# Optimization experiments

Hardware: AMD Instinct MI355X
Metric: run time of the kernel (lower is better)

The kernel has to match this reference:

```python
import jax, jax.numpy as jnp
import numpy as np

N = 50000      # areaNum
E = 64         # embeddingsize
NE = 800000    # nonzeros of normalized adjacency
WK = 9         # walk_length + 1
L = 2          # args.L
TMP = 0.5      # args.choosing_tmp
BIAS = 1e-4


def _logistic_noise(k, shape):
    # eps ~ U(bias, 1-bias); noise = log(eps) - log(1-eps)
    u = jax.random.uniform(k, shape, minval=BIAS, maxval=1.0 - BIAS)
    return jnp.log(u) - jnp.log1p(-u)


def setup_inputs() -> dict:
    key = jax.random.key(0)
    ks = jax.random.split(key, 16)
    rng = np.random.default_rng(0)

    # ---- normalized sparse adjacency (D^-1/2 A D^-1/2), COO sorted by row ----
    row = np.sort(rng.integers(0, N, NE))
    col = rng.integers(0, N, NE)
    deg = np.bincount(row, minlength=N).astype(np.float32)
    dinv = np.where(deg > 0, deg ** -0.5, 0.0).astype(np.float32)
    vals = dinv[row] * dinv[col]

    # ---- random-walk mean-pooling adjacency, row-normalized ----
    rw_row = np.repeat(np.arange(N), WK)
    rw_col = rng.integers(0, N, N * WK)
    rw_col[::WK] = np.arange(N)  # walk starts at self
    rw_vals = np.full(N * WK, 1.0 / WK, dtype=np.float32)

    def lin(k, fan_in, shape):
        return jax.random.normal(k, shape, dtype=jnp.float32) / np.sqrt(fan_in)

    inp = {
        'x': jax.random.normal(ks[0], (N, E), dtype=jnp.float32),
        'vals': jnp.asarray(vals),
        'rw_vals': jnp.asarray(rw_vals),
        't_W1': lin(ks[1], 2 * E, (L, 2 * E, E)),
        't_b1': jnp.zeros((L, E), jnp.float32),
        't_W2': lin(ks[2], E, (L, E, 1)),
        't_b2': jnp.zeros((L, 1), jnp.float32),
        's_W1': lin(ks[3], E, (L, E, E)),
        's_b1': jnp.zeros((L, E), jnp.float32),
        's_W2': lin(ks[4], E, (L, E, 1)),
        's_b2': jnp.zeros((L, 1), jnp.float32),
        't_noise': _logistic_noise(ks[5], (L, NE)),
        's_noise': _logistic_noise(ks[6], (L, N, 1)),
        'row': jnp.asarray(row, dtype=jnp.int64) if jax.config.jax_enable_x64 else jnp.asarray(row, dtype=jnp.int32),
        'col': jnp.asarray(col, dtype=jnp.int32),
        'rw_row': jnp.asarray(rw_row, dtype=jnp.int32),
        'rw_col': jnp.asarray(rw_col, dtype=jnp.int32),
    }
    inp['row'] = jnp.asarray(row, dtype=jnp.int32)
    return inp


def reference(x, vals, rw_vals, t_W1, t_b1, t_W2, t_b2, s_W1, s_b1, s_W2, s_b2,
              t_noise, s_noise, row, col, rw_row, rw_col):
    n = x.shape[0]

    def spmm(r, c, v, h):  # sparse [n,n] @ dense [n,E]
        return jax.ops.segment_sum(v[:, None] * h[c], r, num_segments=n)

    # per-edge concat of ORIGINAL embeddings (same tensor every layer, as in source)
    t_cat = jnp.concatenate([x[row], x[col]], axis=-1)  # [nE, 2E]

    # --- mask-learning pass ---
    cur = x
    t_masks, s_masks = [], []
    for i in range(L):
        cur = spmm(row, col, vals, cur)
        t_h = jax.nn.relu(t_cat @ t_W1[i] + t_b1[i])
        t_logit = t_h @ t_W2[i] + t_b2[i]                      # [nE,1]
        t_m = jax.nn.sigmoid((t_noise[i][:, None] + t_logit) / TMP)[:, 0]
        t_masks.append(t_m)
        s_h = jax.nn.relu(cur @ s_W1[i] + s_b1[i])
        s_logit = s_h @ s_W2[i] + s_b2[i]                      # [N,1]
        s_masks.append(jax.nn.sigmoid((s_noise[i] + s_logit) / TMP))

    # --- t branch: gated spmm propagation, mean over layers ---
    cur_t = x
    acc_t = x
    for i in range(L):
        cur_t = spmm(row, col, vals * t_masks[i], cur_t)
        acc_t = acc_t + cur_t
    emb_t = acc_t / (L + 1)

    # --- s branch: gated mix with random-walk mean pooling, then spmm ---
    cur_s = x
    acc_s = x
    s_reg = jnp.float32(0.0)
    for i in range(L):
        mp = spmm(rw_row, rw_col, rw_vals, cur_s)
        cur_s = s_masks[i] * cur_s + (1.0 - s_masks[i]) * mp
        cur_s = spmm(row, col, vals, cur_s)
        acc_s = acc_s + cur_s
        s_reg = s_reg + s_masks[i].sum() / n
    emb_s = acc_s / (L + 1)
    s_reg = s_reg / L
    t_reg = jnp.float32(0.0)  # source never accumulates into t_reg
    return emb_t, emb_s, t_reg, s_reg, t_masks[-1]
```

## Files before the change

kernel.cpp:

```cpp
#include <hip/hip_runtime.h>

#define NNODES 50000
#define EDIM 64
#define WKLEN 9
#define NEDGE 800000
#define NPAD (NNODES + 64)

using bf16x8 = __attribute__((ext_vector_type(8))) __bf16;
using f32x4  = __attribute__((ext_vector_type(4))) float;

__device__ __align__(256) unsigned short g_xbf[NPAD * EDIM];
__device__ __align__(256) unsigned short g_ABh[NNODES * 128];
__device__ __align__(256) unsigned short g_c1h[NPAD * EDIM];
__device__ __align__(256) unsigned short g_c2h[NPAD * EDIM];
__device__ __align__(256) unsigned short g_g0h[NNODES * EDIM];
__device__ __align__(256) unsigned short g_sc1h[NNODES * EDIM];
__device__ __align__(256) unsigned short g_Pr[NNODES * 128];
__device__ __align__(256) unsigned short g_Pc[NNODES * 128];
__device__ __align__(256) float g_mt0[NEDGE];
__device__ __align__(256) float g_mt1[NEDGE];
__device__ __align__(256) float g_sm0[NNODES];
__device__ __align__(256) float g_sm1[NNODES];
__device__ __align__(256) int   g_rowptr[NNODES + 1];
__device__ __align__(256) unsigned short g_Tswz[2048 * 8];
__device__ __align__(256) unsigned short g_Sswz[1024 * 8];

__device__ __forceinline__ unsigned short f2bf(float f) {
    union { float f; unsigned int i; } v;
    v.f = f;
    unsigned int r = v.i + 0x7FFFu + ((v.i >> 16) & 1u);
    return (unsigned short)(r >> 16);
}
__device__ __forceinline__ float bf2f_lo(unsigned int u) {
    union { unsigned int i; float f; } v; v.i = u << 16; return v.f;
}
__device__ __forceinline__ float bf2f_hi(unsigned int u) {
    union { unsigned int i; float f; } v; v.i = u & 0xFFFF0000u; return v.f;
}

__global__ __launch_bounds__(256) void misc_kernel(
    const float* __restrict__ x, const float* __restrict__ tW1,
    const float* __restrict__ sW1, const int* __restrict__ row,
    int n, int nE)
{
    int bid = blockIdx.x, tid = threadIdx.x;
    if (bid < 1563) {
        int i = bid * 256 + tid;
        if (i < NNODES * EDIM / 8) {
            const float* src = x + i * 8;
            union { unsigned short s[8]; uint4 q; } u;
#pragma unroll
            for (int j = 0; j < 8; ++j) u.s[j] = f2bf(src[j]);
            *(uint4*)&g_xbf[i * 8] = u.q;
        }
    } else if (bid < 1759) {
        int i = (bid - 1563) * 256 + tid;
        if (i > n) return;
        int lo = 0, hi = nE;
        while (lo < hi) {
            int mid = (lo + hi) >> 1;
            if (row[mid] < i) lo = mid + 1; else hi = mid;
        }
        g_rowptr[i] = lo;
    } else if (bid < 1767) {
        int t = (bid - 1759) * 256 + tid;
        int s = t >> 9, f = (t >> 6) & 7, ln = t & 63;
        int li = s >> 1, half = s & 1, ks = f >> 2, nn = f & 3;
        int q = ln >> 4, mcl = ln & 15;
        union { unsigned short sv[8]; uint4 q4; } u;
#pragma unroll
        for (int j = 0; j < 8; ++j) {
            int kg = half * 64 + ks * 32 + q * 8 + j;
            u.sv[j] = f2bf(tW1[li * 8192 + kg * 64 + nn * 16 + mcl]);
        }
        *(uint4*)&g_Tswz[t * 8] = u.q4;
    } else {
        int t = (bid - 1767) * 256 + tid;
        int li = t >> 9, ks = (t >> 8) & 1, nn = (t >> 6) & 3, ln = t & 63;
        int q = ln >> 4, mcl = ln & 15;
        union { unsigned short sv[8]; uint4 q4; } u;
#pragma unroll
        for (int j = 0; j < 8; ++j)
            u.sv[j] = f2bf(sW1[li * 4096 + (ks * 32 + q * 8 + j) * 64 + nn * 16 + mcl]);
        *(uint4*)&g_Sswz[t * 8] = u.q4;
    }
}

__global__ __launch_bounds__(256) void prep2_kernel(int n)
{
// ... 70 lines not shown
        float hB = fmaxf(bf2f_hi(r0[k]) + bf2f_hi(c0[k]) + b1_0[2 * k + 1], 0.f);
        p0 = fmaf(hA, w2_0[2 * k], p0);
        p0 = fmaf(hB, w2_0[2 * k + 1], p0);
        float gA = fmaxf(bf2f_lo(r1[k]) + bf2f_lo(c1[k]) + b1_1[2 * k], 0.f);
        float gB = fmaxf(bf2f_hi(r1[k]) + bf2f_hi(c1[k]) + b1_1[2 * k + 1], 0.f);
        p1 = fmaf(gA, w2_1[2 * k], p1);
        p1 = fmaf(gB, w2_1[2 * k + 1], p1);
    }
#pragma unroll
    for (int off = 1; off <= 4; off <<= 1) {
        p0 += __shfl_xor(p0, off, 64);
        p1 += __shfl_xor(p1, off, 64);
    }
    if (sub == 0) {
        float z0 = (tnoise[e] + p0 + tb2[0]) * 2.0f;
        float m0 = 1.0f / (1.0f + expf(-z0));
        g_mt0[e] = m0;
        float z1 = (tnoise[nE + e] + p1 + tb2[1]) * 2.0f;
        float m1 = 1.0f / (1.0f + expf(-z1));
        g_mt1[e] = m1;
        mask_out[e] = m1;
    }
}

__device__ __forceinline__ void nm_body(
    int bid, const unsigned short* __restrict__ cur, int li,
    const float* __restrict__ b1, const float* __restrict__ W2,
    const float* __restrict__ b2, const float* __restrict__ noise,
    float* __restrict__ smout, int n)
{
    int tid = threadIdx.x;
    int wave = tid >> 6, lane = tid & 63;
    int mc = lane & 15, quad = lane >> 4;
    int nb = bid * 64 + wave * 16;
    const unsigned short* basep = cur + (nb + mc) * 64 + quad * 8;
    bf16x8 af0 = *(const bf16x8*)basep;
    bf16x8 af1 = *(const bf16x8*)(basep + 32);
    f32x4 acc[4];
    const f32x4 zero = {0.f, 0.f, 0.f, 0.f};
#pragma unroll
    for (int nn = 0; nn < 4; ++nn) acc[nn] = zero;
#pragma unroll
    for (int nn = 0; nn < 4; ++nn) {
        bf16x8 b0 = *(const bf16x8*)&g_Sswz[((li * 8 + nn) * 64 + lane) * 8];
        bf16x8 b1f = *(const bf16x8*)&g_Sswz[((li * 8 + 4 + nn) * 64 + lane) * 8];
        acc[nn] = __builtin_amdgcn_mfma_f32_16x16x32_bf16(af0, b0, acc[nn], 0, 0, 0);
        acc[nn] = __builtin_amdgcn_mfma_f32_16x16x32_bf16(af1, b1f, acc[nn], 0, 0, 0);
    }
    float p[4];
#pragma unroll
    for (int r = 0; r < 4; ++r) {
        float s = 0.f;
#pragma unroll
        for (int nn = 0; nn < 4; ++nn) {
            float h = acc[nn][r] + b1[nn * 16 + mc];
            s = fmaf(fmaxf(h, 0.f), W2[nn * 16 + mc], s);
        }
        p[r] = s;
    }
#pragma unroll
    for (int off = 8; off >= 1; off >>= 1)
#pragma unroll
        for (int r = 0; r < 4; ++r) p[r] += __shfl_xor(p[r], off, 64);
    if (mc == 0) {
        float b2v = b2[0];
#pragma unroll
        for (int r = 0; r < 4; ++r) {
            int node = nb + quad * 4 + r;
            if (node < n) {
                float z = (noise[node] + p[r] + b2v) * 2.0f;
                smout[node] = 1.0f / (1.0f + expf(-z));
            }
        }
    }
}

__global__ __launch_bounds__(256) void nm0_kernel(
    const float* __restrict__ sb1, const float* __restrict__ sW2,
    const float* __restrict__ sb2, const float* __restrict__ snz, int n)
{
    nm_body(blockIdx.x, g_c1h, 0, sb1, sW2, sb2, snz, g_sm0, n);
}

__device__ __forceinline__ void s1_process16(
    int sb, int d2, int myc, float myv, float myvm,
    float& p0, float& p1, float& q0, float& q1)
{
    int cc[16]; float vv[16], mm[16]; unsigned uu[16];
#pragma unroll
    for (int k = 0; k < 16; ++k) {
        cc[k] = __shfl(myc, sb + k, 64);
        vv[k] = __shfl(myv, sb + k, 64);
        mm[k] = __shfl(myvm, sb + k, 64);
    }
#pragma unroll
    for (int k = 0; k < 16; ++k)
        uu[k] = *(const unsigned*)&g_xbf[cc[k] * 64 + 2 * d2];
#pragma unroll
    for (int k = 0; k < 16; ++k) {
        p0 = fmaf(vv[k], bf2f_lo(uu[k]), p0);
        p1 = fmaf(vv[k], bf2f_hi(uu[k]), p1);
        q0 = fmaf(mm[k], bf2f_lo(uu[k]), q0);
        q1 = fmaf(mm[k], bf2f_hi(uu[k]), q1);
    }
}

__global__ __launch_bounds__(256) void s1_kernel(
    const int* __restrict__ colv, const float* __restrict__ vals, int n)
{
    int half = threadIdx.x >> 5;
    int w = blockIdx.x * 8 + half;
    int el = half & 1;
    int d2 = threadIdx.x & 31;
    int sb0 = el << 5;
    int s = g_rowptr[w], e = g_rowptr[w + 1];
    float p0 = 0.f, p1 = 0.f, q0 = 0.f, q1 = 0.f;
    for (int base = s; base < e; base += 32) {
        int rem = e - base;
        int myc = 0; float myv = 0.f, myvm = 0.f;
        if (d2 < rem) {
            myc = colv[base + d2];
            myv = vals[base + d2];
            myvm = myv * g_mt0[base + d2];
        }
        s1_process16(sb0, d2, myc, myv, myvm, p0, p1, q0, q1);
        if (rem > 16)
            s1_process16(sb0 + 16, d2, myc, myv, myvm, p0, p1, q0, q1);
    }
    uint2 pk;
    pk.x = (unsigned)f2bf(p0) | ((unsigned)f2bf(q0) << 16);
    pk.y = (unsigned)f2bf(p1) | ((unsigned)f2bf(q1) << 16);
    *(uint2*)&g_ABh[w * 128 + 4 * d2] = pk;
    *(unsigned*)&g_c1h[w * 64 + 2 * d2] =
        (unsigned)f2bf(p0) | ((unsigned)f2bf(p1) << 16);
}

__device__ __forceinline__ void s2_process8(
    int sb, int d2, int myc, float myv, float myvm,
    float& c0, float& c1, float& t0, float& t1)
{
    int cc[8]; float vv[8], mm[8]; uint2 uu[8];
#pragma unroll
    for (int k = 0; k < 8; ++k) {
        cc[k] = __shfl(myc, sb + k, 64);
        vv[k] = __shfl(myv, sb + k, 64);
        mm[k] = __shfl(myvm, sb + k, 64);
    }
#pragma unroll
    for (int k = 0; k < 8; ++k)
        uu[k] = *(const uint2*)&g_ABh[cc[k] * 128 + 4 * d2];
#pragma unroll
    for (int k = 0; k < 8; ++k) {
        c0 = fmaf(vv[k], bf2f_lo(uu[k].x), c0);
        t0 = fmaf(mm[k], bf2f_hi(uu[k].x), t0);
        c1 = fmaf(vv[k], bf2f_lo(uu[k].y), c1);
        t1 = fmaf(mm[k], bf2f_hi(uu[k].y), t1);
    }
}

__device__ __forceinline__ void rw_body(
    int bid, const int* __restrict__ rw_col, const float* __restrict__ rwv,
    const unsigned short* __restrict__ cur, const float* __restrict__ smask,
    unsigned short* __restrict__ outg)
{
    int w = bid * 8 + (threadIdx.x >> 5);
    int d2 = threadIdx.x & 31;
    int base = w * WKLEN;
    float a0 = 0.f, a1 = 0.f;
#pragma unroll
    for (int j = 0; j < WKLEN; ++j) {
        int c = rw_col[base + j];
        float v = rwv[base + j];
        unsigned u = *(const unsigned*)&cur[c * 64 + 2 * d2];
        a0 = fmaf(v, bf2f_lo(u), a0);
        a1 = fmaf(v, bf2f_hi(u), a1);
    }
    float sm = smask[w];
    unsigned u = *(const unsigned*)&cur[w * 64 + 2 * d2];
    float r0 = sm * bf2f_lo(u) + (1.f - sm) * a0;
    float r1 = sm * bf2f_hi(u) + (1.f - sm) * a1;
    *(unsigned*)&outg[w * 64 + 2 * d2] =
        (unsigned)f2bf(r0) | ((unsigned)f2bf(r1) << 16);
}

__global__ __launch_bounds__(256) void s2_rw0_kernel(
    const int* __restrict__ colv, const float* __restrict__ vals,
    const int* __restrict__ rw_col, const float* __restrict__ rwv,
    const float* __restrict__ x, float* __restrict__ emb_t, int n)
{
    if (blockIdx.x >= 6250) {
        rw_body(blockIdx.x - 6250, rw_col, rwv, g_xbf, g_sm0, g_g0h);
        return;
    }
    int half = threadIdx.x >> 5;
    int w = blockIdx.x * 8 + half;
    int el = half & 1;
    int d2 = threadIdx.x & 31;
    int sb0 = el << 5;
    int s = g_rowptr[w], e = g_rowptr[w + 1];
    float c0 = 0.f, c1 = 0.f, t0 = 0.f, t1 = 0.f;
    for (int base = s; base < e; base += 32) {
        int rem = e - base;
        int myc = 0; float myv = 0.f, myvm = 0.f;
        if (d2 < rem) {
            myc = colv[base + d2];
            myv = vals[base + d2];
            myvm = myv * g_mt1[base + d2];
        }
        s2_process8(sb0, d2, myc, myv, myvm, c0, c1, t0, t1);
        if (rem > 8)  s2_process8(sb0 + 8,  d2, myc, myv, myvm, c0, c1, t0, t1);
        if (rem > 16) s2_process8(sb0 + 16, d2, myc, myv, myvm, c0, c1, t0, t1);
        if (rem > 24) s2_process8(sb0 + 24, d2, myc, myv, myvm, c0, c1, t0, t1);
    }
    int o2 = w * 64 + 2 * d2;
    uint2 U2v = *(const uint2*)&g_ABh[w * 128 + 4 * d2];
    float2 et;
    et.x = (x[o2]     + bf2f_hi(U2v.x) + t0) * (1.0f / 3.0f);
    et.y = (x[o2 + 1] + bf2f_hi(U2v.y) + t1) * (1.0f / 3.0f);
    *(float2*)&emb_t[o2] = et;
    *(unsigned*)&g_c2h[o2] = (unsigned)f2bf(c0) | ((unsigned)f2bf(c1) << 16);
}

__device__ __forceinline__ void sp_process16(
    const unsigned short* __restrict__ h, int sb, int d2,
    int myc, float myv, float& a0, float& a1)
{
    int cc[16]; float vv[16]; unsigned uu[16];
#pragma unroll
    for (int k = 0; k < 16; ++k) {
        cc[k] = __shfl(myc, sb + k, 64);
        vv[k] = __shfl(myv, sb + k, 64);
    }
#pragma unroll
    for (int k = 0; k < 16; ++k)
        uu[k] = *(const unsigned*)&h[cc[k] * 64 + 2 * d2];
#pragma unroll
    for (int k = 0; k < 16; ++k) {
        a0 = fmaf(vv[k], bf2f_lo(uu[k]), a0);
        a1 = fmaf(vv[k], bf2f_hi(uu[k]), a1);
    }
}

__device__ __forceinline__ void spmm_body(
    int bid, const int* __restrict__ colv, const float* __restrict__ vals,
    const unsigned short* __restrict__ h, float* __restrict__ l0,
    float* __restrict__ l1, int* __restrict__ wout, int* __restrict__ d2out)
{
    int half = threadIdx.x >> 5;
    int w = bid * 8 + half;
    int el = half & 1;
    int d2 = threadIdx.x & 31;
    int sb0 = el << 5;
    int s = g_rowptr[w], e = g_rowptr[w + 1];
    float a0 = 0.f, a1 = 0.f;
    for (int base = s; base < e; base += 32) {
        int rem = e - base;
        int myc = 0; float myv = 0.f;
        if (d2 < rem) {
            myc = colv[base + d2];
            myv = vals[base + d2];
        }
        sp_process16(h, sb0, d2, myc, myv, a0, a1);
        if (rem > 16) sp_process16(h, sb0 + 16, d2, myc, myv, a0, a1);
    }
    *l0 = a0; *l1 = a1; *wout = w; *d2out = d2;
}

__global__ __launch_bounds__(256) void spmm10_nm1_kernel(
    const int* __restrict__ colv, const float* __restrict__ vals,
    const float* __restrict__ sb1, const float* __restrict__ sW2,
    const float* __restrict__ sb2, const float* __restrict__ snz, int n)
{
    if (blockIdx.x >= 6250) {
        nm_body(blockIdx.x - 6250, g_c2h, 1, sb1, sW2, sb2, snz, g_sm1, n);
        return;
    }
    float a0, a1; int w, d2;
    spmm_body(blockIdx.x, colv, vals, g_g0h, &a0, &a1, &w, &d2);
    *(unsigned*)&g_sc1h[w * 64 + 2 * d2] =
        (unsigned)f2bf(a0) | ((unsigned)f2bf(a1) << 16);
}

__global__ __launch_bounds__(256) void rw1_kernel(
    const int* __restrict__ rw_col, const float* __restrict__ rwv)
{
    rw_body(blockIdx.x, rw_col, rwv, g_sc1h, g_sm1, g_g0h);
}

__global__ __launch_bounds__(256) void spmm12_fin_kernel(
    const int* __restrict__ colv, const float* __restrict__ vals,
    const float* __restrict__ x, float* __restrict__ emb_s,
    float* __restrict__ out, int n)
{
    if (blockIdx.x >= 6250) {
        __shared__ float red[256];
        float s = 0.f;
        for (int i = threadIdx.x; i < n; i += 256) s += g_sm0[i] + g_sm1[i];
        red[threadIdx.x] = s;
        __syncthreads();
        for (int off = 128; off >= 1; off >>= 1) {
            if (threadIdx.x < off) red[threadIdx.x] += red[threadIdx.x + off];
            __syncthreads();
        }
        if (threadIdx.x == 0) {
            out[6400000] = 0.0f;
            out[6400001] = red[0] / (2.0f * n);
        }
        return;
    }
    float a0, a1; int w, d2;
    spmm_body(blockIdx.x, colv, vals, g_g0h, &a0, &a1, &w, &d2);
    int o2 = w * 64 + 2 * d2;
    unsigned uc = *(const unsigned*)&g_sc1h[o2];
    float2 es;
    es.x = (x[o2]     + bf2f_lo(uc) + a0) * (1.0f / 3.0f);
    es.y = (x[o2 + 1] + bf2f_hi(uc) + a1) * (1.0f / 3.0f);
    *(float2*)&emb_s[o2] = es;
}

extern "C" void kernel_launch(void* const* d_in, const int* in_sizes, int n_in,
                              void* d_out, int out_size, void* d_ws, size_t ws_size,
                              hipStream_t stream)
{
    const float* x    = (const float*)d_in[0];
    const float* vals = (const float*)d_in[1];
    const float* rwv  = (const float*)d_in[2];
    const float* tW1  = (const float*)d_in[3];
    const float* tb1  = (const float*)d_in[4];
    const float* tW2  = (const float*)d_in[5];
    const float* tb2  = (const float*)d_in[6];
    const float* sW1  = (const float*)d_in[7];
    const float* sb1  = (const float*)d_in[8];
    const float* sW2  = (const float*)d_in[9];
    const float* sb2  = (const float*)d_in[10];
    const float* tnz  = (const float*)d_in[11];
    const float* snz  = (const float*)d_in[12];
    const int* row   = (const int*)d_in[13];
    const int* colv  = (const int*)d_in[14];
    const int* rwcol = (const int*)d_in[16];

    const int n = NNODES;
    const int nE = in_sizes[1];

    float* out   = (float*)d_out;
    float* emb_t = out;
    float* emb_s = out + 3200000;
    float* masko = out + 6400002;

    misc_kernel<<<1771, 256, 0, stream>>>(x, tW1, sW1, row, n, nE);
    prep2_kernel<<<782, 256, 0, stream>>>(n);
    edge_mask_kernel<<<nE / 32, 256, 0, stream>>>(tb1, tW2, tb2, tnz,
                                                  row, colv, masko, nE);
    s1_kernel<<<6250, 256, 0, stream>>>(colv, vals, n);
    nm0_kernel<<<782, 256, 0, stream>>>(sb1, sW2, sb2, snz, n);
    s2_rw0_kernel<<<12500, 256, 0, stream>>>(colv, vals, rwcol, rwv, x, emb_t, n);
    spmm10_nm1_kernel<<<6250 + 782, 256, 0, stream>>>(colv, vals,
                                                      sb1 + 64, sW2 + 64, sb2 + 1,
                                                      snz + n, n);
    rw1_kernel<<<6250, 256, 0, stream>>>(rwcol, rwv);
    spmm12_fin_kernel<<<6251, 256, 0, stream>>>(colv, vals, x, emb_s, out, n);
}
```

Baseline: 335.8 us.

## Batch gather loads ahead of FMAs in SpMM kernels and grid-stride the final SpMM

The SpMM and random-walk gather loops now issue all 32 (or 9) neighbor loads together, fenced by sched_barrier, before the shuffles and FMAs. This raises memory-level parallelism per wave. Launch bounds now request 2 blocks per SM. The final emb_s SpMM uses a grid-stride loop over 1250 blocks instead of 6250, so the reduction block starts sooner. The trade-off is higher register pressure from the 32-entry arrays, which could lower occupancy or cause spills.

New measurement: 347.2 us. 3.4% more time.

```diff
diff --git a/kernel.cpp b/kernel.cpp
--- a/kernel.cpp
+++ b/kernel.cpp
@@ -5,6 +5,9 @@
 #define WKLEN 9
 #define NEDGE 800000
 #define NPAD (NNODES + 64)
+
+#define NGRP 6250
+#define FINGS 1250
 
 using bf16x8 = __attribute__((ext_vector_type(8))) __bf16;
 using f32x4  = __attribute__((ext_vector_type(4))) float;
@@ -241,30 +244,7 @@
     nm_body(blockIdx.x, g_c1h, 0, sb1, sW2, sb2, snz, g_sm0, n);
 }
 
-__device__ __forceinline__ void s1_process16(
-    int sb, int d2, int myc, float myv, float myvm,
-    float& p0, float& p1, float& q0, float& q1)
-{
-    int cc[16]; float vv[16], mm[16]; unsigned uu[16];
-#pragma unroll
-    for (int k = 0; k < 16; ++k) {
-        cc[k] = __shfl(myc, sb + k, 64);
-        vv[k] = __shfl(myv, sb + k, 64);
-        mm[k] = __shfl(myvm, sb + k, 64);
-    }
-#pragma unroll
-    for (int k = 0; k < 16; ++k)
-        uu[k] = *(const unsigned*)&g_xbf[cc[k] * 64 + 2 * d2];
-#pragma unroll
-    for (int k = 0; k < 16; ++k) {
-        p0 = fmaf(vv[k], bf2f_lo(uu[k]), p0);
-        p1 = fmaf(vv[k], bf2f_hi(uu[k]), p1);
-        q0 = fmaf(mm[k], bf2f_lo(uu[k]), q0);
-        q1 = fmaf(mm[k], bf2f_hi(uu[k]), q1);
-    }
-}
-
-__global__ __launch_bounds__(256) void s1_kernel(
+__global__ __launch_bounds__(256, 2) void s1_kernel(
     const int* __restrict__ colv, const float* __restrict__ vals, int n)
 {
     int half = threadIdx.x >> 5;
@@ -282,9 +262,35 @@
             myv = vals[base + d2];
             myvm = myv * g_mt0[base + d2];
         }
-        s1_process16(sb0, d2, myc, myv, myvm, p0, p1, q0, q1);
-        if (rem > 16)
-            s1_process16(sb0 + 16, d2, myc, myv, myvm, p0, p1, q0, q1);
+        int cc[32]; unsigned uu[32];
+#pragma unroll
+        for (int k = 0; k < 32; ++k) cc[k] = __shfl(myc, sb0 + k, 64);
+        __builtin_amdgcn_sched_barrier(0);
+#pragma unroll
+        for (int k = 0; k < 16; ++k)
+            uu[k] = *(const unsigned*)&g_xbf[cc[k] * 64 + 2 * d2];
+        if (rem > 16) {
+#pragma unroll
+            for (int k = 16; k < 32; ++k)
+                uu[k] = *(const unsigned*)&g_xbf[cc[k] * 64 + 2 * d2];
+        } else {
+#pragma unroll
+            for (int k = 16; k < 32; ++k) uu[k] = 0u;
+        }
+        __builtin_amdgcn_sched_barrier(0);
+        float vv[32], mm[32];
+#pragma unroll
+        for (int k = 0; k < 32; ++k) {
+            vv[k] = __shfl(myv, sb0 + k, 64);
+            mm[k] = __shfl(myvm, sb0 + k, 64);
+        }
+#pragma unroll
+        for (int k = 0; k < 32; ++k) {
+            p0 = fmaf(vv[k], bf2f_lo(uu[k]), p0);
+            p1 = fmaf(vv[k], bf2f_hi(uu[k]), p1);
+            q0 = fmaf(mm[k], bf2f_lo(uu[k]), q0);
+            q1 = fmaf(mm[k], bf2f_hi(uu[k]), q1);
+        }
     }
     uint2 pk;
     pk.x = (unsigned)f2bf(p0) | ((unsigned)f2bf(q0) << 16);
@@ -294,29 +300,6 @@
         (unsigned)f2bf(p0) | ((unsigned)f2bf(p1) << 16);
 }
 
-__device__ __forceinline__ void s2_process8(
-    int sb, int d2, int myc, float myv, float myvm,
-    float& c0, float& c1, float& t0, float& t1)
-{
-    int cc[8]; float vv[8], mm[8]; uint2 uu[8];
-#pragma unroll
-    for (int k = 0; k < 8; ++k) {
-        cc[k] = __shfl(myc, sb + k, 64);
-        vv[k] = __shfl(myv, sb + k, 64);
-        mm[k] = __shfl(myvm, sb + k, 64);
-    }
-#pragma unroll
-    for (int k = 0; k < 8; ++k)
-        uu[k] = *(const uint2*)&g_ABh[cc[k] * 128 + 4 * d2];
-#pragma unroll
-    for (int k = 0; k < 8; ++k) {
-        c0 = fmaf(vv[k], bf2f_lo(uu[k].x), c0);
-        t0 = fmaf(mm[k], bf2f_hi(uu[k].x), t0);
-        c1 = fmaf(vv[k], bf2f_lo(uu[k].y), c1);
-        t1 = fmaf(mm[k], bf2f_hi(uu[k].y), t1);
-    }
-}
-
 __device__ __forceinline__ void rw_body(
     int bid, const int* __restrict__ rw_col, const float* __restrict__ rwv,
     const unsigned short* __restrict__ cur, const float* __restrict__ smask,
@@ -325,24 +308,32 @@
     int w = bid * 8 + (threadIdx.x >> 5);
     int d2 = threadIdx.x & 31;
     int base = w * WKLEN;
+    int cc[WKLEN]; float vv[WKLEN]; unsigned uu[WKLEN];
+#pragma unroll
+    for (int j = 0; j < WKLEN; ++j) {
+        cc[j] = rw_col[base + j];
+        vv[j] = rwv[base + j];
+    }
+    __builtin_amdgcn_sched_barrier(0);
+#pragma unroll
+    for (int j = 0; j < WKLEN; ++j)
+        uu[j] = *(const unsigned*)&cur[cc[j] * 64 + 2 * d2];
+    unsigned us = *(const unsigned*)&cur[w * 64 + 2 * d2];
+    __builtin_amdgcn_sched_barrier(0);
     float a0 = 0.f, a1 = 0.f;
 #pragma unroll
     for (int j = 0; j < WKLEN; ++j) {
-        int c = rw_col[base + j];
-        float v = rwv[base + j];
-        unsigned u = *(const unsigned*)&cur[c * 64 + 2 * d2];
-        a0 = fmaf(v, bf2f_lo(u), a0);
-        a1 = fmaf(v, bf2f_hi(u), a1);
+        a0 = fmaf(vv[j], bf2f_lo(uu[j]), a0);
+        a1 = fmaf(vv[j], bf2f_hi(uu[j]), a1);
     }
     float sm = smask[w];
-    unsigned u = *(const unsigned*)&cur[w * 64 + 2 * d2];
-    float r0 = sm * bf2f_lo(u) + (1.f - sm) * a0;
-    float r1 = sm * bf2f_hi(u) + (1.f - sm) * a1;
+    float r0 = sm * bf2f_lo(us) + (1.f - sm) * a0;
+    float r1 = sm * bf2f_hi(us) + (1.f - sm) * a1;
     *(unsigned*)&outg[w * 64 + 2 * d2] =
         (unsigned)f2bf(r0) | ((unsigned)f2bf(r1) << 16);
 }
 
-__global__ __launch_bounds__(256) void s2_rw0_kernel(
+__global__ __launch_bounds__(256, 2) void s2_rw0_kernel(
     const int* __restrict__ colv, const float* __restrict__ vals,
     const int* __restrict__ rw_col, const float* __restrict__ rwv,
     const float* __restrict__ x, float* __restrict__ emb_t, int n)
@@ -366,10 +357,35 @@
             myv = vals[base + d2];
             myvm = myv * g_mt1[base + d2];
         }
-        s2_process8(sb0, d2, myc, myv, myvm, c0, c1, t0, t1);
-        if (rem > 8)  s2_process8(sb0 + 8,  d2, myc, myv, myvm, c0, c1, t0, t1);
-        if (rem > 16) s2_process8(sb0 + 16, d2, myc, myv, myvm, c0, c1, t0, t1);
-        if (rem > 24) s2_process8(sb0 + 24, d2, myc, myv, myvm, c0, c1, t0, t1);
+        int cc[32]; uint2 uu[32];
+#pragma unroll
+        for (int k = 0; k < 32; ++k) cc[k] = __shfl(myc, sb0 + k, 64);
+        __builtin_amdgcn_sched_barrier(0);
+#pragma unroll
+        for (int k = 0; k < 16; ++k)
+            uu[k] = *(const uint2*)&g_ABh[cc[k] * 128 + 4 * d2];
+        if (rem > 16) {
+#pragma unroll
+            for (int k = 16; k < 32; ++k)
+                uu[k] = *(const uint2*)&g_ABh[cc[k] * 128 + 4 * d2];
+        } else {
+#pragma unroll
+            for (int k = 16; k < 32; ++k) { uu[k].x = 0u; uu[k].y = 0u; }
+        }
+        __builtin_amdgcn_sched_barrier(0);
+        float vv[32], mm[32];
+#pragma unroll
+        for (int k = 0; k < 32; ++k) {
+            vv[k] = __shfl(myv, sb0 + k, 64);
+            mm[k] = __shfl(myvm, sb0 + k, 64);
+        }
+#pragma unroll
+        for (int k = 0; k < 32; ++k) {
+            c0 = fmaf(vv[k], bf2f_lo(uu[k].x), c0);
+            t0 = fmaf(mm[k], bf2f_hi(uu[k].x), t0);
+            c1 = fmaf(vv[k], bf2f_lo(uu[k].y), c1);
+            t1 = fmaf(mm[k], bf2f_hi(uu[k].y), t1);
+        }
     }
     int o2 = w * 64 + 2 * d2;
     uint2 U2v = *(const uint2*)&g_ABh[w * 128 + 4 * d2];
@@ -378,26 +394,6 @@
     et.y = (x[o2 + 1] + bf2f_hi(U2v.y) + t1) * (1.0f / 3.0f);
     *(float2*)&emb_t[o2] = et;
     *(unsigned*)&g_c2h[o2] = (unsigned)f2bf(c0) | ((unsigned)f2bf(c1) << 16);
-}
-
-__device__ __forceinline__ void sp_process16(
-    const unsigned short* __restrict__ h, int sb, int d2,
-    int myc, float myv, float& a0, float& a1)
-{
-    int cc[16]; float vv[16]; unsigned uu[16];
-#pragma unroll
-    for (int k = 0; k < 16; ++k) {
-        cc[k] = __shfl(myc, sb + k, 64);
-        vv[k] = __shfl(myv, sb + k, 64);
-    }
-#pragma unroll
-    for (int k = 0; k < 16; ++k)
-        uu[k] = *(const unsigned*)&h[cc[k] * 64 + 2 * d2];
-#pragma unroll
-    for (int k = 0; k < 16; ++k) {
-        a0 = fmaf(vv[k], bf2f_lo(uu[k]), a0);
-        a1 = fmaf(vv[k], bf2f_hi(uu[k]), a1);
-    }
 }
 
 __device__ __forceinline__ void spmm_body(
@@ -419,13 +415,35 @@
             myc = colv[base + d2];
             myv = vals[base + d2];
         }
-        sp_process16(h, sb0, d2, myc, myv, a0, a1);
-        if (rem > 16) sp_process16(h, sb0 + 16, d2, myc, myv, a0, a1);
+        int cc[32]; unsigned uu[32];
+#pragma unroll
+        for (int k = 0; k < 32; ++k) cc[k] = __shfl(myc, sb0 + k, 64);
+        __builtin_amdgcn_sched_barrier(0);
+#pragma unroll
+        for (int k = 0; k < 16; ++k)
+            uu[k] = *(const unsigned*)&h[cc[k] * 64 + 2 * d2];
+        if (rem > 16) {
+#pragma unroll
+            for (int k = 16; k < 32; ++k)
+                uu[k] = *(const unsigned*)&h[cc[k] * 64 + 2 * d2];
+        } else {
+#pragma unroll
+            for (int k = 16; k < 32; ++k) uu[k] = 0u;
+        }
+        __builtin_amdgcn_sched_barrier(0);
+        float vv[32];
+#pragma unroll
+        for (int k = 0; k < 32; ++k) vv[k] = __shfl(myv, sb0 + k, 64);
+#pragma unroll
+        for (int k = 0; k < 32; ++k) {
+            a0 = fmaf(vv[k], bf2f_lo(uu[k]), a0);
+            a1 = fmaf(vv[k], bf2f_hi(uu[k]), a1);
+        }
     }
     *l0 = a0; *l1 = a1; *wout = w; *d2out = d2;
 }
 
-__global__ __launch_bounds__(256) void spmm10_nm1_kernel(
+__global__ __launch_bounds__(256, 2) void spmm10_nm1_kernel(
     const int* __restrict__ colv, const float* __restrict__ vals,
     const float* __restrict__ sb1, const float* __restrict__ sW2,
     const float* __restrict__ sb2, const float* __restrict__ snz, int n)
@@ -440,18 +458,18 @@
         (unsigned)f2bf(a0) | ((unsigned)f2bf(a1) << 16);
 }
 
-__global__ __launch_bounds__(256) void rw1_kernel(
+__global__ __launch_bounds__(256, 2) void rw1_kernel(
     const int* __restrict__ rw_col, const float* __restrict__ rwv)
 {
     rw_body(blockIdx.x, rw_col, rwv, g_sc1h, g_sm1, g_g0h);
 }
 
-__global__ __launch_bounds__(256) void spmm12_fin_kernel(
+__global__ __launch_bounds__(256, 2) void spmm12_fin_kernel(
     const int* __restrict__ colv, const float* __restrict__ vals,
     const float* __restrict__ x, float* __restrict__ emb_s,
     float* __restrict__ out, int n)
 {
-    if (blockIdx.x >= 6250) {
+    if (blockIdx.x >= FINGS) {
         __shared__ float red[256];
         float s = 0.f;
         for (int i = threadIdx.x; i < n; i += 256) s += g_sm0[i] + g_sm1[i];
@@ -467,14 +485,16 @@
         }
         return;
     }
-    float a0, a1; int w, d2;
-    spmm_body(blockIdx.x, colv, vals, g_g0h, &a0, &a1, &w, &d2);
-    int o2 = w * 64 + 2 * d2;
-    unsigned uc = *(const unsigned*)&g_sc1h[o2];
-    float2 es;
-    es.x = (x[o2]     + bf2f_lo(uc) + a0) * (1.0f / 3.0f);
-    es.y = (x[o2 + 1] + bf2f_hi(uc) + a1) * (1.0f / 3.0f);
-    *(float2*)&emb_s[o2] = es;
+    for (int vb = blockIdx.x; vb < NGRP; vb += FINGS) {
+        float a0, a1; int w, d2;
+        spmm_body(vb, colv, vals, g_g0h, &a0, &a1, &w, &d2);
+        int o2 = w * 64 + 2 * d2;
+        unsigned uc = *(const unsigned*)&g_sc1h[o2];
+        float2 es;
+        es.x = (x[o2]     + bf2f_lo(uc) + a0) * (1.0f / 3.0f);
+        es.y = (x[o2 + 1] + bf2f_hi(uc) + a1) * (1.0f / 3.0f);
+        *(float2*)&emb_s[o2] = es;
+    }
 }
 
 extern "C" void kernel_launch(void* const* d_in, const int* in_sizes, int n_in,
@@ -513,9 +533,9 @@
     s1_kernel<<<6250, 256, 0, stream>>>(colv, vals, n);
     nm0_kernel<<<782, 256, 0, stream>>>(sb1, sW2, sb2, snz, n);
     s2_rw0_kernel<<<12500, 256, 0, stream>>>(colv, vals, rwcol, rwv, x, emb_t, n);
-    spmm10_nm1_kernel<<<6250 + 782, 256, 0, stream>>>(colv, vals,
-                                                      sb1 + 64, sW2 + 64, sb2 + 1,
-                                                      snz + n, n);
+    spmm10_nm1_kernel<<<7032, 256, 0, stream>>>(colv, vals,
+                                                sb1 + 64, sW2 + 64, sb2 + 1,
+                                                snz + n, n);
     rw1_kernel<<<6250, 256, 0, stream>>>(rwcol, rwv);
-    spmm12_fin_kernel<<<6251, 256, 0, stream>>>(colv, vals, x, emb_s, out, n);
-}
+    spmm12_fin_kernel<<<FINGS + 1, 256, 0, stream>>>(colv, vals, x, emb_s, out, n);
+}
```

## Assign one wave per row with 16-byte gathers and cross-lane reduction in SpMM kernels

Applied to the files above, without the earlier changes.

The gather kernels (s1, s2, spmm, random-walk) change from half-wave-per-row with shuffle-broadcast of column indices to a full wave per row. Lane groups handle different edges in parallel and each lane loads 16 bytes of the feature row, and partial sums are combined with xor-shuffles at the end. The aim is more memory-level parallelism per gather and wider vector loads in place of 4-byte loads. In exchange, twice as many blocks are launched, a reduction is added at the end of each row, and only one lane group does the stores.

Result: slower. 377.3 us (+12.3%).

```diff
diff --git a/kernel.cpp b/kernel.cpp
--- a/kernel.cpp
+++ b/kernel.cpp
@@ -5,6 +5,8 @@
 #define WKLEN 9
 #define NEDGE 800000
 #define NPAD (NNODES + 64)
+
+#define NBLK 12500
 
 using bf16x8 = __attribute__((ext_vector_type(8))) __bf16;
 using f32x4  = __attribute__((ext_vector_type(4))) float;
@@ -241,105 +243,117 @@
     nm_body(blockIdx.x, g_c1h, 0, sb1, sW2, sb2, snz, g_sm0, n);
 }
 
-__device__ __forceinline__ void s1_process16(
-    int sb, int d2, int myc, float myv, float myvm,
-    float& p0, float& p1, float& q0, float& q1)
-{
-    int cc[16]; float vv[16], mm[16]; unsigned uu[16];
-#pragma unroll
-    for (int k = 0; k < 16; ++k) {
-        cc[k] = __shfl(myc, sb + k, 64);
-        vv[k] = __shfl(myv, sb + k, 64);
-        mm[k] = __shfl(myvm, sb + k, 64);
-    }
-#pragma unroll
-    for (int k = 0; k < 16; ++k)
-        uu[k] = *(const unsigned*)&g_xbf[cc[k] * 64 + 2 * d2];
-#pragma unroll
-    for (int k = 0; k < 16; ++k) {
-        p0 = fmaf(vv[k], bf2f_lo(uu[k]), p0);
-        p1 = fmaf(vv[k], bf2f_hi(uu[k]), p1);
-        q0 = fmaf(mm[k], bf2f_lo(uu[k]), q0);
-        q1 = fmaf(mm[k], bf2f_hi(uu[k]), q1);
-    }
-}
-
 __global__ __launch_bounds__(256) void s1_kernel(
     const int* __restrict__ colv, const float* __restrict__ vals, int n)
 {
-    int half = threadIdx.x >> 5;
-    int w = blockIdx.x * 8 + half;
-    int el = half & 1;
-    int d2 = threadIdx.x & 31;
-    int sb0 = el << 5;
+    int lane = threadIdx.x & 63;
+    int eg = lane >> 3, sl = lane & 7;
+    int w = blockIdx.x * 4 + (threadIdx.x >> 6);
     int s = g_rowptr[w], e = g_rowptr[w + 1];
-    float p0 = 0.f, p1 = 0.f, q0 = 0.f, q1 = 0.f;
+    float ap[8], aq[8];
+#pragma unroll
+    for (int j = 0; j < 8; ++j) { ap[j] = 0.f; aq[j] = 0.f; }
     for (int base = s; base < e; base += 32) {
-        int rem = e - base;
-        int myc = 0; float myv = 0.f, myvm = 0.f;
-        if (d2 < rem) {
-            myc = colv[base + d2];
-            myv = vals[base + d2];
-            myvm = myv * g_mt0[base + d2];
-        }
-        s1_process16(sb0, d2, myc, myv, myvm, p0, p1, q0, q1);
-        if (rem > 16)
-            s1_process16(sb0 + 16, d2, myc, myv, myvm, p0, p1, q0, q1);
-    }
-    uint2 pk;
-    pk.x = (unsigned)f2bf(p0) | ((unsigned)f2bf(q0) << 16);
-    pk.y = (unsigned)f2bf(p1) | ((unsigned)f2bf(q1) << 16);
-    *(uint2*)&g_ABh[w * 128 + 4 * d2] = pk;
-    *(unsigned*)&g_c1h[w * 64 + 2 * d2] =
-        (unsigned)f2bf(p0) | ((unsigned)f2bf(p1) << 16);
-}
-
-__device__ __forceinline__ void s2_process8(
-    int sb, int d2, int myc, float myv, float myvm,
-    float& c0, float& c1, float& t0, float& t1)
-{
-    int cc[8]; float vv[8], mm[8]; uint2 uu[8];
-#pragma unroll
-    for (int k = 0; k < 8; ++k) {
-        cc[k] = __shfl(myc, sb + k, 64);
-        vv[k] = __shfl(myv, sb + k, 64);
-        mm[k] = __shfl(myvm, sb + k, 64);
-    }
-#pragma unroll
-    for (int k = 0; k < 8; ++k)
-        uu[k] = *(const uint2*)&g_ABh[cc[k] * 128 + 4 * d2];
-#pragma unroll
-    for (int k = 0; k < 8; ++k) {
-        c0 = fmaf(vv[k], bf2f_lo(uu[k].x), c0);
-        t0 = fmaf(mm[k], bf2f_hi(uu[k].x), t0);
-        c1 = fmaf(vv[k], bf2f_lo(uu[k].y), c1);
-        t1 = fmaf(mm[k], bf2f_hi(uu[k].y), t1);
+        int ci[4]; float vi[4], mi[4];
+#pragma unroll
+        for (int j = 0; j < 4; ++j) {
+            int idx = base + j * 8 + eg;
+            bool ok = idx < e;
+            ci[j] = ok ? colv[idx] : 0;
+            float v = ok ? vals[idx] : 0.f;
+            vi[j] = v;
+            mi[j] = ok ? v * g_mt0[idx] : 0.f;
+        }
+        uint4 uu[4];
+#pragma unroll
+        for (int j = 0; j < 4; ++j)
+            uu[j] = *(const uint4*)&g_xbf[ci[j] * 64 + sl * 8];
+#pragma unroll
+        for (int j = 0; j < 4; ++j) {
+            float f0 = bf2f_lo(uu[j].x), f1 = bf2f_hi(uu[j].x);
+            float f2 = bf2f_lo(uu[j].y), f3 = bf2f_hi(uu[j].y);
+            float f4 = bf2f_lo(uu[j].z), f5 = bf2f_hi(uu[j].z);
+            float f6 = bf2f_lo(uu[j].w), f7 = bf2f_hi(uu[j].w);
+            ap[0] = fmaf(vi[j], f0, ap[0]); aq[0] = fmaf(mi[j], f0, aq[0]);
+            ap[1] = fmaf(vi[j], f1, ap[1]); aq[1] = fmaf(mi[j], f1, aq[1]);
+            ap[2] = fmaf(vi[j], f2, ap[2]); aq[2] = fmaf(mi[j], f2, aq[2]);
+            ap[3] = fmaf(vi[j], f3, ap[3]); aq[3] = fmaf(mi[j], f3, aq[3]);
+            ap[4] = fmaf(vi[j], f4, ap[4]); aq[4] = fmaf(mi[j], f4, aq[4]);
+            ap[5] = fmaf(vi[j], f5, ap[5]); aq[5] = fmaf(mi[j], f5, aq[5]);
+            ap[6] = fmaf(vi[j], f6, ap[6]); aq[6] = fmaf(mi[j], f6, aq[6]);
+            ap[7] = fmaf(vi[j], f7, ap[7]); aq[7] = fmaf(mi[j], f7, aq[7]);
+        }
+    }
+#pragma unroll
+    for (int m = 8; m <= 32; m <<= 1)
+#pragma unroll
+        for (int j = 0; j < 8; ++j) {
+            ap[j] += __shfl_xor(ap[j], m, 64);
+            aq[j] += __shfl_xor(aq[j], m, 64);
+        }
+    if (eg == 0) {
+        uint4 A, B;
+        A.x = (unsigned)f2bf(ap[0]) | ((unsigned)f2bf(aq[0]) << 16);
+        A.y = (unsigned)f2bf(ap[1]) | ((unsigned)f2bf(aq[1]) << 16);
+        A.z = (unsigned)f2bf(ap[2]) | ((unsigned)f2bf(aq[2]) << 16);
+        A.w = (unsigned)f2bf(ap[3]) | ((unsigned)f2bf(aq[3]) << 16);
+        B.x = (unsigned)f2bf(ap[4]) | ((unsigned)f2bf(aq[4]) << 16);
+        B.y = (unsigned)f2bf(ap[5]) | ((unsigned)f2bf(aq[5]) << 16);
+        B.z = (unsigned)f2bf(ap[6]) | ((unsigned)f2bf(aq[6]) << 16);
+        B.w = (unsigned)f2bf(ap[7]) | ((unsigned)f2bf(aq[7]) << 16);
+        *(uint4*)&g_ABh[w * 128 + 16 * sl] = A;
+        *(uint4*)&g_ABh[w * 128 + 16 * sl + 8] = B;
+        uint4 C;
+        C.x = (unsigned)f2bf(ap[0]) | ((unsigned)f2bf(ap[1]) << 16);
+        C.y = (unsigned)f2bf(ap[2]) | ((unsigned)f2bf(ap[3]) << 16);
+        C.z = (unsigned)f2bf(ap[4]) | ((unsigned)f2bf(ap[5]) << 16);
+        C.w = (unsigned)f2bf(ap[6]) | ((unsigned)f2bf(ap[7]) << 16);
+        *(uint4*)&g_c1h[w * 64 + 8 * sl] = C;
     }
 }
 
 __device__ __forceinline__ void rw_body(
-    int bid, const int* __restrict__ rw_col, const float* __restrict__ rwv,
+    int w, const int* __restrict__ rw_col, const float* __restrict__ rwv,
     const unsigned short* __restrict__ cur, const float* __restrict__ smask,
     unsigned short* __restrict__ outg)
 {
-    int w = bid * 8 + (threadIdx.x >> 5);
-    int d2 = threadIdx.x & 31;
+    int lane = threadIdx.x & 63;
+    int eg = lane >> 3, sl = lane & 7;
     int base = w * WKLEN;
-    float a0 = 0.f, a1 = 0.f;
-#pragma unroll
-    for (int j = 0; j < WKLEN; ++j) {
-        int c = rw_col[base + j];
-        float v = rwv[base + j];
-        unsigned u = *(const unsigned*)&cur[c * 64 + 2 * d2];
-        a0 = fmaf(v, bf2f_lo(u), a0);
-        a1 = fmaf(v, bf2f_hi(u), a1);
-    }
+    int c1 = rw_col[base + eg];
+    float v1 = rwv[base + eg];
+    int c9 = rw_col[base + 8];
+    float v9 = (eg == 0) ? rwv[base + 8] : 0.f;
+    uint4 u1 = *(const uint4*)&cur[c1 * 64 + sl * 8];
+    uint4 u9 = *(const uint4*)&cur[c9 * 64 + sl * 8];
+    uint4 us = *(const uint4*)&cur[w * 64 + sl * 8];
+    float a[8];
+    a[0] = v1 * bf2f_lo(u1.x) + v9 * bf2f_lo(u9.x);
+    a[1] = v1 * bf2f_hi(u1.x) + v9 * bf2f_hi(u9.x);
+    a[2] = v1 * bf2f_lo(u1.y) + v9 * bf2f_lo(u9.y);
+    a[3] = v1 * bf2f_hi(u1.y) + v9 * bf2f_hi(u9.y);
+    a[4] = v1 * bf2f_lo(u1.z) + v9 * bf2f_lo(u9.z);
+    a[5] = v1 * bf2f_hi(u1.z) + v9 * bf2f_hi(u9.z);
+    a[6] = v1 * bf2f_lo(u1.w) + v9 * bf2f_lo(u9.w);
+    a[7] = v1 * bf2f_hi(u1.w) + v9 * bf2f_hi(u9.w);
+#pragma unroll
+    for (int m = 8; m <= 32; m <<= 1)
+#pragma unroll
+        for (int j = 0; j < 8; ++j) a[j] += __shfl_xor(a[j], m, 64);
     float sm = smask[w];
-    unsigned u = *(const unsigned*)&cur[w * 64 + 2 * d2];
-    float r0 = sm * bf2f_lo(u) + (1.f - sm) * a0;
-    float r1 = sm * bf2f_hi(u) + (1.f - sm) * a1;
-    *(unsigned*)&outg[w * 64 + 2 * d2] =
-        (unsigned)f2bf(r0) | ((unsigned)f2bf(r1) << 16);
+    float sf[8] = { bf2f_lo(us.x), bf2f_hi(us.x), bf2f_lo(us.y), bf2f_hi(us.y),
+                    bf2f_lo(us.z), bf2f_hi(us.z), bf2f_lo(us.w), bf2f_hi(us.w) };
+    float r[8];
+#pragma unroll
+    for (int j = 0; j < 8; ++j) r[j] = sm * sf[j] + (1.f - sm) * a[j];
+    if (eg == 0) {
+        uint4 O;
+        O.x = (unsigned)f2bf(r[0]) | ((unsigned)f2bf(r[1]) << 16);
+        O.y = (unsigned)f2bf(r[2]) | ((unsigned)f2bf(r[3]) << 16);
+        O.z = (unsigned)f2bf(r[4]) | ((unsigned)f2bf(r[5]) << 16);
+        O.w = (unsigned)f2bf(r[6]) | ((unsigned)f2bf(r[7]) << 16);
+        *(uint4*)&outg[w * 64 + 8 * sl] = O;
+    }
 }
 
 __global__ __launch_bounds__(256) void s2_rw0_kernel(
@@ -347,82 +361,105 @@
     const int* __restrict__ rw_col, const float* __restrict__ rwv,
     const float* __restrict__ x, float* __restrict__ emb_t, int n)
 {
-    if (blockIdx.x >= 6250) {
-        rw_body(blockIdx.x - 6250, rw_col, rwv, g_xbf, g_sm0, g_g0h);
+    int lane = threadIdx.x & 63;
+    if (blockIdx.x >= NBLK) {
+        int w = (blockIdx.x - NBLK) * 4 + (threadIdx.x >> 6);
+        rw_body(w, rw_col, rwv, g_xbf, g_sm0, g_g0h);
         return;
     }
-    int half = threadIdx.x >> 5;
-    int w = blockIdx.x * 8 + half;
-    int el = half & 1;
-    int d2 = threadIdx.x & 31;
-    int sb0 = el << 5;
+    int eg = lane >> 4, sl = lane & 15;
+    int w = blockIdx.x * 4 + (threadIdx.x >> 6);
     int s = g_rowptr[w], e = g_rowptr[w + 1];
-    float c0 = 0.f, c1 = 0.f, t0 = 0.f, t1 = 0.f;
+    float ac[4], at[4];
+#pragma unroll
+    for (int j = 0; j < 4; ++j) { ac[j] = 0.f; at[j] = 0.f; }
+    for (int base = s; base < e; base += 16) {
+        int ci[4]; float vi[4], mi[4];
+#pragma unroll
+        for (int j = 0; j < 4; ++j) {
+            int idx = base + j * 4 + eg;
+            bool ok = idx < e;
+            ci[j] = ok ? colv[idx] : 0;
+            float v = ok ? vals[idx] : 0.f;
+            vi[j] = v;
+            mi[j] = ok ? v * g_mt1[idx] : 0.f;
+        }
+        uint4 uu[4];
+#pragma unroll
+        for (int j = 0; j < 4; ++j)
+            uu[j] = *(const uint4*)&g_ABh[ci[j] * 128 + sl * 8];
+#pragma unroll
+        for (int j = 0; j < 4; ++j) {
+            ac[0] = fmaf(vi[j], bf2f_lo(uu[j].x), ac[0]);
+            at[0] = fmaf(mi[j], bf2f_hi(uu[j].x), at[0]);
+            ac[1] = fmaf(vi[j], bf2f_lo(uu[j].y), ac[1]);
+            at[1] = fmaf(mi[j], bf2f_hi(uu[j].y), at[1]);
+            ac[2] = fmaf(vi[j], bf2f_lo(uu[j].z), ac[2]);
+            at[2] = fmaf(mi[j], bf2f_hi(uu[j].z), at[2]);
+            ac[3] = fmaf(vi[j], bf2f_lo(uu[j].w), ac[3]);
+            at[3] = fmaf(mi[j], bf2f_hi(uu[j].w), at[3]);
+        }
+    }
+#pragma unroll
+    for (int m = 16; m <= 32; m <<= 1)
+#pragma unroll
+        for (int j = 0; j < 4; ++j) {
+            ac[j] += __shfl_xor(ac[j], m, 64);
+            at[j] += __shfl_xor(at[j], m, 64);
+        }
+    if (eg == 0) {
+        int o = w * 64 + 4 * sl;
+        uint4 Uv = *(const uint4*)&g_ABh[w * 128 + sl * 8];
+        float4 xv = *(const float4*)&x[o];
+        float4 et;
+        et.x = (xv.x + bf2f_hi(Uv.x) + at[0]) * (1.0f / 3.0f);
+        et.y = (xv.y + bf2f_hi(Uv.y) + at[1]) * (1.0f / 3.0f);
+        et.z = (xv.z + bf2f_hi(Uv.z) + at[2]) * (1.0f / 3.0f);
+        et.w = (xv.w + bf2f_hi(Uv.w) + at[3]) * (1.0f / 3.0f);
+        *(float4*)&emb_t[o] = et;
+        uint2 ch;
+        ch.x = (unsigned)f2bf(ac[0]) | ((unsigned)f2bf(ac[1]) << 16);
+        ch.y = (unsigned)f2bf(ac[2]) | ((unsigned)f2bf(ac[3]) << 16);
+        *(uint2*)&g_c2h[o] = ch;
+    }
+}
+
+__device__ __forceinline__ void spmm_row_wave(
+    int w, const int* __restrict__ colv, const float* __restrict__ vals,
+    const unsigned short* __restrict__ h, float acc[8], int eg, int sl)
+{
+    int s = g_rowptr[w], e = g_rowptr[w + 1];
+#pragma unroll
+    for (int j = 0; j < 8; ++j) acc[j] = 0.f;
     for (int base = s; base < e; base += 32) {
-        int rem = e - base;
-        int myc = 0; float myv = 0.f, myvm = 0.f;
-        if (d2 < rem) {
-            myc = colv[base + d2];
-            myv = vals[base + d2];
-            myvm = myv * g_mt1[base + d2];
-        }
-        s2_process8(sb0, d2, myc, myv, myvm, c0, c1, t0, t1);
-        if (rem > 8)  s2_process8(sb0 + 8,  d2, myc, myv, myvm, c0, c1, t0, t1);
-        if (rem > 16) s2_process8(sb0 + 16, d2, myc, myv, myvm, c0, c1, t0, t1);
-        if (rem > 24) s2_process8(sb0 + 24, d2, myc, myv, myvm, c0, c1, t0, t1);
-    }
-    int o2 = w * 64 + 2 * d2;
-    uint2 U2v = *(const uint2*)&g_ABh[w * 128 + 4 * d2];
-    float2 et;
-    et.x = (x[o2]     + bf2f_hi(U2v.x) + t0) * (1.0f / 3.0f);
-    et.y = (x[o2 + 1] + bf2f_hi(U2v.y) + t1) * (1.0f / 3.0f);
-    *(float2*)&emb_t[o2] = et;
-    *(unsigned*)&g_c2h[o2] = (unsigned)f2bf(c0) | ((unsigned)f2bf(c1) << 16);
-}
-
-__device__ __forceinline__ void sp_process16(
-    const unsigned short* __restrict__ h, int sb, int d2,
-    int myc, float myv, float& a0, float& a1)
-{
-    int cc[16]; float vv[16]; unsigned uu[16];
-#pragma unroll
-    for (int k = 0; k < 16; ++k) {
-        cc[k] = __shfl(myc, sb + k, 64);
-        vv[k] = __shfl(myv, sb + k, 64);
-    }
-#pragma unroll
-    for (int k = 0; k < 16; ++k)
-        uu[k] = *(const unsigned*)&h[cc[k] * 64 + 2 * d2];
-#pragma unroll
-    for (int k = 0; k < 16; ++k) {
-        a0 = fmaf(vv[k], bf2f_lo(uu[k]), a0);
-        a1 = fmaf(vv[k], bf2f_hi(uu[k]), a1);
-    }
-}
-
-__device__ __forceinline__ void spmm_body(
-    int bid, const int* __restrict__ colv, const float* __restrict__ vals,
-    const unsigned short* __restrict__ h, float* __restrict__ l0,
-    float* __restrict__ l1, int* __restrict__ wout, int* __restrict__ d2out)
-{
-    int half = threadIdx.x >> 5;
-    int w = bid * 8 + half;
-    int el = half & 1;
-    int d2 = threadIdx.x & 31;
-    int sb0 = el << 5;
-    int s = g_rowptr[w], e = g_rowptr[w + 1];
-    float a0 = 0.f, a1 = 0.f;
-    for (int base = s; base < e; base += 32) {
-        int rem = e - base;
-        int myc = 0; float myv = 0.f;
-        if (d2 < rem) {
-            myc = colv[base + d2];
-            myv = vals[base + d2];
-        }
-        sp_process16(h, sb0, d2, myc, myv, a0, a1);
-        if (rem > 16) sp_process16(h, sb0 + 16, d2, myc, myv, a0, a1);
-    }
-    *l0 = a0; *l1 = a1; *wout = w; *d2out = d2;
+        int ci[4]; float vi[4];
+#pragma unroll
+        for (int j = 0; j < 4; ++j) {
+            int idx = base + j * 8 + eg;
+            bool ok = idx < e;
+            ci[j] = ok ? colv[idx] : 0;
+            vi[j] = ok ? vals[idx] : 0.f;
+        }
+        uint4 uu[4];
+#pragma unroll
+        for (int j = 0; j < 4; ++j)
+            uu[j] = *(const uint4*)&h[ci[j] * 64 + sl * 8];
+#pragma unroll
+        for (int j = 0; j < 4; ++j) {
+            acc[0] = fmaf(vi[j], bf2f_lo(uu[j].x), acc[0]);
+            acc[1] = fmaf(vi[j], bf2f_hi(uu[j].x), acc[1]);
+            acc[2] = fmaf(vi[j], bf2f_lo(uu[j].y), acc[2]);
+            acc[3] = fmaf(vi[j], bf2f_hi(uu[j].y), acc[3]);
+            acc[4] = fmaf(vi[j], bf2f_lo(uu[j].z), acc[4]);
+            acc[5] = fmaf(vi[j], bf2f_hi(uu[j].z), acc[5]);
+            acc[6] = fmaf(vi[j], bf2f_lo(uu[j].w), acc[6]);
+            acc[7] = fmaf(vi[j], bf2f_hi(uu[j].w), acc[7]);
+        }
+    }
+#pragma unroll
+    for (int m = 8; m <= 32; m <<= 1)
+#pragma unroll
+        for (int j = 0; j < 8; ++j) acc[j] += __shfl_xor(acc[j], m, 64);
 }
 
 __global__ __launch_bounds__(256) void spmm10_nm1_kernel(
@@ -430,20 +467,30 @@
     const float* __restrict__ sb1, const float* __restrict__ sW2,
     const float* __restrict__ sb2, const float* __restrict__ snz, int n)
 {
-    if (blockIdx.x >= 6250) {
-        nm_body(blockIdx.x - 6250, g_c2h, 1, sb1, sW2, sb2, snz, g_sm1, n);
+    if (blockIdx.x >= NBLK) {
+        nm_body(blockIdx.x - NBLK, g_c2h, 1, sb1, sW2, sb2, snz, g_sm1, n);
         return;
     }
-    float a0, a1; int w, d2;
-    spmm_body(blockIdx.x, colv, vals, g_g0h, &a0, &a1, &w, &d2);
-    *(unsigned*)&g_sc1h[w * 64 + 2 * d2] =
-        (unsigned)f2bf(a0) | ((unsigned)f2bf(a1) << 16);
+    int lane = threadIdx.x & 63;
+    int eg = lane >> 3, sl = lane & 7;
+    int w = blockIdx.x * 4 + (threadIdx.x >> 6);
+    float a[8];
+    spmm_row_wave(w, colv, vals, g_g0h, a, eg, sl);
+    if (eg == 0) {
+        uint4 O;
+        O.x = (unsigned)f2bf(a[0]) | ((unsigned)f2bf(a[1]) << 16);
+        O.y = (unsigned)f2bf(a[2]) | ((unsigned)f2bf(a[3]) << 16);
+        O.z = (unsigned)f2bf(a[4]) | ((unsigned)f2bf(a[5]) << 16);
+        O.w = (unsigned)f2bf(a[6]) | ((unsigned)f2bf(a[7]) << 16);
+        *(uint4*)&g_sc1h[w * 64 + 8 * sl] = O;
+    }
 }
 
 __global__ __launch_bounds__(256) void rw1_kernel(
     const int* __restrict__ rw_col, const float* __restrict__ rwv)
 {
-    rw_body(blockIdx.x, rw_col, rwv, g_sc1h, g_sm1, g_g0h);
+    int w = blockIdx.x * 4 + (threadIdx.x >> 6);
+    rw_body(w, rw_col, rwv, g_sc1h, g_sm1, g_g0h);
 }
 
 __global__ __launch_bounds__(256) void spmm12_fin_kernel(
@@ -451,7 +498,7 @@
     const float* __restrict__ x, float* __restrict__ emb_s,
     float* __restrict__ out, int n)
 {
-    if (blockIdx.x >= 6250) {
+    if (blockIdx.x >= NBLK) {
         __shared__ float red[256];
         float s = 0.f;
         for (int i = threadIdx.x; i < n; i += 256) s += g_sm0[i] + g_sm1[i];
@@ -467,14 +514,28 @@
         }
         return;
     }
-    float a0, a1; int w, d2;
-    spmm_body(blockIdx.x, colv, vals, g_g0h, &a0, &a1, &w, &d2);
-    int o2 = w * 64 + 2 * d2;
-    unsigned uc = *(const unsigned*)&g_sc1h[o2];
-    float2 es;
-    es.x = (x[o2]     + bf2f_lo(uc) + a0) * (1.0f / 3.0f);
-    es.y = (x[o2 + 1] + bf2f_hi(uc) + a1) * (1.0f / 3.0f);
-    *(float2*)&emb_s[o2] = es;
+    int lane = threadIdx.x & 63;
+    int eg = lane >> 3, sl = lane & 7;
+    int w = blockIdx.x * 4 + (threadIdx.x >> 6);
+    float a[8];
+    spmm_row_wave(w, colv, vals, g_g0h, a, eg, sl);
+    if (eg == 0) {
+        int o = w * 64 + 8 * sl;
+        uint4 uc = *(const uint4*)&g_sc1h[o];
+        float4 xa = *(const float4*)&x[o];
+        float4 xb = *(const float4*)&x[o + 4];
+        float4 ea, eb;
+        ea.x = (xa.x + bf2f_lo(uc.x) + a[0]) * (1.0f / 3.0f);
+        ea.y = (xa.y + bf2f_hi(uc.x) + a[1]) * (1.0f / 3.0f);
+        ea.z = (xa.z + bf2f_lo(uc.y) + a[2]) * (1.0f / 3.0f);
+        ea.w = (xa.w + bf2f_hi(uc.y) + a[3]) * (1.0f / 3.0f);
+        eb.x = (xb.x + bf2f_lo(uc.z) + a[4]) * (1.0f / 3.0f);
+        eb.y = (xb.y + bf2f_hi(uc.z) + a[5]) * (1.0f / 3.0f);
+        eb.z = (xb.z + bf2f_lo(uc.w) + a[6]) * (1.0f / 3.0f);
+        eb.w = (xb.w + bf2f_hi(uc.w) + a[7]) * (1.0f / 3.0f);
+        *(float4*)&emb_s[o] = ea;
+        *(float4*)&emb_s[o + 4] = eb;
+    }
 }
 
 extern "C" void kernel_launch(void* const* d_in, const int* in_sizes, int n_in,
@@ -510,12 +571,12 @@
     prep2_kernel<<<782, 256, 0, stream>>>(n);
     edge_mask_kernel<<<nE / 32, 256, 0, stream>>>(tb1, tW2, tb2, tnz,
                                                   row, colv, masko, nE);
-    s1_kernel<<<6250, 256, 0, stream>>>(colv, vals, n);
+    s1_kernel<<<NBLK, 256, 0, stream>>>(colv, vals, n);
     nm0_kernel<<<782, 256, 0, stream>>>(sb1, sW2, sb2, snz, n);
-    s2_rw0_kernel<<<12500, 256, 0, stream>>>(colv, vals, rwcol, rwv, x, emb_t, n);
-    spmm10_nm1_kernel<<<6250 + 782, 256, 0, stream>>>(colv, vals,
+    s2_rw0_kernel<<<2 * NBLK, 256, 0, stream>>>(colv, vals, rwcol, rwv, x, emb_t, n);
+    spmm10_nm1_kernel<<<NBLK + 782, 256, 0, stream>>>(colv, vals,
                                                       sb1 + 64, sW2 + 64, sb2 + 1,
                                                       snz + n, n);
-    rw1_kernel<<<6250, 256, 0, stream>>>(rwcol, rwv);
-    spmm12_fin_kernel<<<6251, 256, 0, stream>>>(colv, vals, x, emb_s, out, n);
-}
+    rw1_kernel<<<NBLK, 256, 0, stream>>>(rwcol, rwv);
+    spmm12_fin_kernel<<<NBLK + 1, 256, 0, stream>>>(colv, vals, x, emb_s, out, n);
+}
```
